# Kernel optimization log

Measured on AMD Instinct MI355X. Metric: run time of the kernel, lower is better.

The kernel has to match this reference:

```python
import jax, jax.numpy as jnp
import numpy as np

N_USERS = 100000
N_ITEMS = 100000
EMB = 64
N_NODES = N_USERS + N_ITEMS + 2  # +1 padding row each for users and items
N_EDGES = 1200000
N_BEHAVIORS = 3
LAYERS = [3, 3, 3]
EPS = 1e-12  # F.normalize eps


def setup_inputs() -> dict:
    key = jax.random.key(0)
    k1, k2, k3, k4, k5 = jax.random.split(key, 5)
    user_emb = jax.random.normal(k1, (N_USERS + 1, EMB), dtype=jnp.float32)
    item_emb = jax.random.normal(k2, (N_ITEMS + 1, EMB), dtype=jnp.float32)
    rows = jax.random.randint(k3, (N_BEHAVIORS, N_EDGES), 0, N_NODES, dtype=jnp.int32)
    cols = jax.random.randint(k4, (N_BEHAVIORS, N_EDGES), 0, N_NODES, dtype=jnp.int32)
    weights = jax.random.uniform(k5, (N_BEHAVIORS, N_EDGES), dtype=jnp.float32)
    return {"user_emb": user_emb, "item_emb": item_emb, "rows": rows,
            "cols": cols, "weights": weights}


def _spmm(rows_b, cols_b, w_b, x):
    # sparse [N,N] @ dense [N,D] via gather + segment-sum (COO SpMM)
    msg = x[cols_b] * w_b[:, None]                      # [E, D]
    return jax.ops.segment_sum(msg, rows_b, num_segments=N_NODES)


def _l2_normalize(x):
    norm = jnp.sqrt(jnp.sum(x * x, axis=-1, keepdims=True))
    return x / jnp.maximum(norm, EPS)


def reference(user_emb, item_emb, rows, cols, weights):
    # NSED.gcn_propagate: sequential LightGCN per behavior with residual chaining
    total = jnp.concatenate([user_emb, item_emb], axis=0)  # [N, D]
    outs = []
    for b in range(N_BEHAVIORS):
        x = total
        acc = x            # running sum of layer embeddings (== mean of stack)
        for _ in range(LAYERS[b]):
            x = _spmm(rows[b], cols[b], weights[b], x)
            acc = acc + x
        lightgcn_emb = acc / jnp.float32(LAYERS[b] + 1)    # stack+mean over layers
        total = _l2_normalize(lightgcn_emb) + total
        outs.append(total)
    return jnp.stack(outs, axis=0)  # [B, N, D]
```

## Files before the change

kernel.cpp:

```cpp
#include <hip/hip_runtime.h>
#include <math.h>

#define N_USERS 100000
#define N_ITEMS 100000
#define EMB 64
#define N_NODES (N_USERS + N_ITEMS + 2)
#define N_EDGES 1200000
#define E3 (3 * N_EDGES)
#define N3 (3 * N_NODES)
#define ND ((long)N_NODES * (long)EMB)

#define KPB 2048
#define NBUCKET ((N3 + KPB - 1) / KPB)
#define CAP 13056
#define EPB 8192
#define SCT 512
#define NB_P1 ((E3 + EPB - 1) / EPB)

typedef float f32x4 __attribute__((ext_vector_type(4)));
typedef float f32x8 __attribute__((ext_vector_type(8)));
typedef unsigned short u16x4 __attribute__((ext_vector_type(4)));
typedef unsigned short u16x8 __attribute__((ext_vector_type(8)));

__device__ inline unsigned short f2bf(float f) {
    unsigned int u = __float_as_uint(f);
    return (unsigned short)((u + 0x7FFFu + ((u >> 16) & 1u)) >> 16);
}
__device__ inline void fma8(f32x8& acc, float w, u16x8 s) {
    #pragma unroll
    for (int j = 0; j < 8; ++j)
        acc[j] = fmaf(w, __uint_as_float((unsigned int)s[j] << 16), acc[j]);
}
__device__ inline f32x8 bf8_to_f8(u16x8 s) {
    f32x8 f;
    #pragma unroll
    for (int j = 0; j < 8; ++j) f[j] = __uint_as_float((unsigned int)s[j] << 16);
    return f;
}
__device__ inline u16x8 f8_to_bf8(f32x8 f) {
    u16x8 s;
    #pragma unroll
    for (int j = 0; j < 8; ++j) s[j] = f2bf(f[j]);
    return s;
}

__global__ void make_tb_kernel(const float4* __restrict__ u,
                               const float4* __restrict__ it,
                               u16x4* __restrict__ tb) {
    long i = (long)blockIdx.x * blockDim.x + threadIdx.x;
    if (i >= ND / 4) return;
    long n = i >> 4;
    float4 v = (n < (long)(N_USERS + 1)) ? u[i] : it[i - (long)(N_USERS + 1) * 16];
    u16x4 b;
    b.x = f2bf(v.x); b.y = f2bf(v.y); b.z = f2bf(v.z); b.w = f2bf(v.w);
    tb[i] = b;
}

__global__ void init_bcur_kernel(int* __restrict__ bcur, unsigned int* __restrict__ sedge) {
    int i = blockIdx.x * blockDim.x + threadIdx.x;
    if (i < NBUCKET) bcur[i] = i * CAP;
    if (i < 16) sedge[E3 + i] = 0u;
}

__global__ void bucket_scatter_kernel(const int* __restrict__ rows,
                                      const int* __restrict__ cols,
                                      const float* __restrict__ w,
                                      int* __restrict__ bcur,
                                      int2* __restrict__ tmpedge) {
    __shared__ int h[NBUCKET];
    __shared__ int lbase[NBUCKET];
    for (int i = threadIdx.x; i < NBUCKET; i += SCT) h[i] = 0;
    __syncthreads();
    long base = (long)blockIdx.x * EPB;
    int keys[EPB / SCT];
    for (int k = 0; k < EPB / SCT; ++k) {
        long e = base + k * SCT + threadIdx.x;
        int key = -1;
        if (e < E3) {
            int b = (e >= 2L * N_EDGES) ? 2 : ((e >= N_EDGES) ? 1 : 0);
            key = b * N_NODES + rows[e];
            atomicAdd(&h[key / KPB], 1);
        }
        keys[k] = key;
    }
    __syncthreads();
    for (int i = threadIdx.x; i < NBUCKET; i += SCT) {
        int c = h[i];
        lbase[i] = c ? atomicAdd(&bcur[i], c) : 0;
        h[i] = 0;
    }
    __syncthreads();
    for (int k = 0; k < EPB / SCT; ++k) {
        long e = base + k * SCT + threadIdx.x;
        int key = keys[k];
        if (key >= 0) {
            int bk = key / KPB;
            int pos = lbase[bk] + atomicAdd(&h[bk], 1);
            int2 pk;
            pk.x = ((key & (KPB - 1)) << 18) | cols[e];
            pk.y = __float_as_int(w[e]);
            tmpedge[pos] = pk;
        }
    }
}

__global__ void bucket_scan_kernel(const int* __restrict__ bcur, int* __restrict__ bbase,
                                   int* __restrict__ rowptr) {
    __shared__ int sm[1024];
    __shared__ int carry;
    int tid = threadIdx.x;
    if (tid == 0) carry = 0;
    __syncthreads();
    for (int base = 0; base < NBUCKET; base += 1024) {
        int i = base + tid;
        int v = (i < NBUCKET) ? (bcur[i] - i * CAP) : 0;
        sm[tid] = v;
        __syncthreads();
        for (int off = 1; off < 1024; off <<= 1) {
            int t = (tid >= off) ? sm[tid - off] : 0;
            __syncthreads();
            sm[tid] += t;
            __syncthreads();
        }
        if (i < NBUCKET) bbase[i] = sm[tid] - v + carry;
        __syncthreads();
        if (tid == 0) carry += sm[1023];
        __syncthreads();
    }
    if (tid == 0) { bbase[NBUCKET] = E3; rowptr[N3] = E3; }
}

__global__ void bucket_sort_kernel(const int* __restrict__ bbase,
                                   const int2* __restrict__ tmpedge,
                                   unsigned int* __restrict__ sedge,
                                   int* __restrict__ rowptr) {
    int g = blockIdx.x;
    int s = bbase[g];
    int cnt = bbase[g + 1] - s;
    long tb = (long)g * CAP;
    __shared__ int h[KPB];
    __shared__ int ex[KPB];
    __shared__ int tmp[512];
    int tid = threadIdx.x;
    #pragma unroll
    for (int j = 0; j < 4; ++j) h[tid * 4 + j] = 0;
    __syncthreads();
    for (int i = tid; i < cnt; i += 512) atomicAdd(&h[tmpedge[tb + i].x >> 18], 1);
    __syncthreads();
    int a0 = h[tid * 4], a1 = h[tid * 4 + 1], a2 = h[tid * 4 + 2], a3 = h[tid * 4 + 3];
    int psum = a0 + a1 + a2 + a3;
    tmp[tid] = psum;
    __syncthreads();
    for (int off = 1; off < 512; off <<= 1) {
        int t = (tid >= off) ? tmp[tid - off] : 0;
        __syncthreads();
        tmp[tid] += t;
        __syncthreads();
    }
    int pex = tmp[tid] - psum;
    ex[tid * 4]     = pex;
    ex[tid * 4 + 1] = pex + a0;
    ex[tid * 4 + 2] = pex + a0 + a1;
    ex[tid * 4 + 3] = pex + a0 + a1 + a2;
    __syncthreads();
    for (int j = tid; j < KPB; j += 512) {
        int key = g * KPB + j;
        if (key < N3) rowptr[key] = s + ex[j];
    }
    #pragma unroll
    for (int j = 0; j < 4; ++j) h[tid * 4 + j] = ex[tid * 4 + j];
    __syncthreads();
    for (int i = tid; i < cnt; i += 512) {
        int2 pk = tmpedge[tb + i];
        int kl = pk.x >> 18;
        int pos = s + atomicAdd(&h[kl], 1);
        float w = __int_as_float(pk.y);
        int wq = (int)fmaf(w, 16384.f, 0.5f);
        wq = wq > 16383 ? 16383 : (wq < 0 ? 0 : wq);
        sedge[pos] = ((unsigned int)(pk.x & 0x3FFFF) << 14) | (unsigned int)wq;
    }
}

__global__ void spmm_bf16_kernel(const int* __restrict__ rowptr,
                                 const unsigned int* __restrict__ sedge,
                                 const u16x8* __restrict__ x,
                                 u16x8* __restrict__ y) {
    int wid  = threadIdx.x >> 6;
    int lane = threadIdx.x & 63;
    int r = lane >> 3;
    int q = lane & 7;
    int n = (blockIdx.x * 4 + wid) * 8 + r;
    if (n >= N_NODES) return;
    int s = rowptr[n], e = rowptr[n + 1];
    f32x8 acc = {0.f, 0.f, 0.f, 0.f, 0.f, 0.f, 0.f, 0.f};
    for (int base = s; ; base += 8) {
        unsigned int ee[8];
        u16x8 bb[8];
        float ww[8];
        #pragma unroll
        for (int j = 0; j < 8; ++j) ee[j] = sedge[base + j];
        #pragma unroll
        for (int j = 0; j < 8; ++j) {
            bool valid = (base + j) < e;
            int c = valid ? (int)(ee[j] >> 14) : 0;
            ww[j] = valid ? (float)(ee[j] & 16383u) * (1.0f / 16384.0f) : 0.f;
            bb[j] = x[(long)c * 8 + q];
        }
        #pragma unroll
        for (int j = 0; j < 8; ++j) fma8(acc, ww[j], bb[j]);
        if (base + 8 >= e) break;
    }
    __builtin_nontemporal_store(f8_to_bf8(acc), &y[(long)n * 8 + q]);
}

__global__ void spmm_final_kernel(const int* __restrict__ rowptr,
                                  const unsigned int* __restrict__ sedge,
                                  const u16x8* __restrict__ Qb,
                                  const float* __restrict__ Tin,
                                  const float* __restrict__ uemb,
                                  const float* __restrict__ iemb,
                                  const u16x8* __restrict__ Pb,
                                  float* __restrict__ outp,
                                  u16x8* __restrict__ TbOut) {
    int wid  = threadIdx.x >> 6;
    int lane = threadIdx.x & 63;
    int r = lane >> 3;
    int q = lane & 7;
    int n = (blockIdx.x * 4 + wid) * 8 + r;
    if (n >= N_NODES) return;
    int s = rowptr[n], e = rowptr[n + 1];
    f32x8 acc = {0.f, 0.f, 0.f, 0.f, 0.f, 0.f, 0.f, 0.f};
    for (int base = s; ; base += 8) {
        unsigned int ee[8];
        u16x8 bb[8];
        float ww[8];
        #pragma unroll
        for (int j = 0; j < 8; ++j) ee[j] = sedge[base + j];
        #pragma unroll
        for (int j = 0; j < 8; ++j) {
            bool valid = (base + j) < e;
            int c = valid ? (int)(ee[j] >> 14) : 0;
            ww[j] = valid ? (float)(ee[j] & 16383u) * (1.0f / 16384.0f) : 0.f;
            bb[j] = Qb[(long)c * 8 + q];
        }
        #pragma unroll
        for (int j = 0; j < 8; ++j) fma8(acc, ww[j], bb[j]);
        if (base + 8 >= e) break;
    }
    const float* tsrc;
    if (Tin) tsrc = Tin + (long)n * EMB;
    else if (n <= N_USERS) tsrc = uemb + (long)n * EMB;
    else tsrc = iemb + (long)(n - N_USERS - 1) * EMB;
    long o = (long)n * 8 + q;
    f32x8 t = *(const f32x8*)(tsrc + q * 8);
    f32x8 p = bf8_to_f8(Pb[o]);
    f32x8 qv = bf8_to_f8(Qb[o]);
    f32x8 v;
    float ss = 0.f;
    #pragma unroll
    for (int j = 0; j < 8; ++j) {
        v[j] = (t[j] + p[j] + qv[j] + acc[j]) * 0.25f;
        ss = fmaf(v[j], v[j], ss);
    }
    ss += __shfl_xor(ss, 1, 64);
    ss += __shfl_xor(ss, 2, 64);
    ss += __shfl_xor(ss, 4, 64);
    float inv = 1.0f / fmaxf(sqrtf(ss), 1e-12f);
    f32x8 ov;
    #pragma unroll
    for (int j = 0; j < 8; ++j) ov[j] = fmaf(v[j], inv, t[j]);
    __builtin_nontemporal_store(ov, (f32x8*)(outp + (long)n * EMB + q * 8));
    if (TbOut) __builtin_nontemporal_store(f8_to_bf8(ov), &TbOut[o]);
}

extern "C" void kernel_launch(void* const* d_in, const int* in_sizes, int n_in,
                              void* d_out, int out_size, void* d_ws, size_t ws_size,
                              hipStream_t stream) {
    const float* user_emb = (const float*)d_in[0];
    const float* item_emb = (const float*)d_in[1];
    const int*   rows     = (const int*)d_in[2];
    const int*   cols     = (const int*)d_in[3];
    const float* weights  = (const float*)d_in[4];
    float* out = (float*)d_out;

    unsigned short* Tb   = (unsigned short*)d_ws;
    unsigned short* Pq   = Tb + ND;
    unsigned short* Qq   = Pq + ND;
    int2* tmpedge = (int2*)(Qq + ND);
    unsigned int* sedge = (unsigned int*)(tmpedge + (long)NBUCKET * CAP);
    int*  rowptr  = (int*)(sedge + E3 + 16);
    int*  bbase   = rowptr + N3 + 2;
    int*  bcur    = bbase + NBUCKET + 2;

    float* o0 = out;
    float* o1 = out + ND;
    float* o2 = out + 2 * ND;

    const long v4_blocks  = (ND / 4 + 255) / 256;
    const long row_blocks = ((long)N_NODES + 31) / 32;

    init_bcur_kernel<<<(NBUCKET + 255) / 256, 256, 0, stream>>>(bcur, sedge);
    bucket_scatter_kernel<<<NB_P1, SCT, 0, stream>>>(rows, cols, weights, bcur, tmpedge);
    bucket_scan_kernel<<<1, 1024, 0, stream>>>(bcur, bbase, rowptr);
    bucket_sort_kernel<<<NBUCKET, 512, 0, stream>>>(bbase, tmpedge, sedge, rowptr);

    make_tb_kernel<<<v4_blocks, 256, 0, stream>>>((const float4*)user_emb,
                                                  (const float4*)item_emb, (u16x4*)Tb);

    const float* Tins[3] = { nullptr, o0, o1 };
    float*       Dsts[3] = { o0, o1, o2 };

    for (int b = 0; b < 3; ++b) {
        const int* rp = rowptr + (long)b * N_NODES;
        u16x8* Pb = (u16x8*)Pq;
        u16x8* Qb = (u16x8*)Qq;

        spmm_bf16_kernel<<<row_blocks, 256, 0, stream>>>(rp, sedge, (const u16x8*)Tb, Pb);
        spmm_bf16_kernel<<<row_blocks, 256, 0, stream>>>(rp, sedge, (const u16x8*)Pb, Qb);
        spmm_final_kernel<<<row_blocks, 256, 0, stream>>>(rp, sedge, (const u16x8*)Qb,
                                                          Tins[b], user_emb, item_emb,
                                                          (const u16x8*)Pb, Dsts[b],
                                                          (b < 2) ? (u16x8*)Tb : nullptr);
    }
}
```

Measured before the change: 417.0 us.

## Replace CSR edge layout with fixed-width ELL plus overflow buffer

Converts the sorted CSR edge list into an ELL layout of 16 slots per row, with edges beyond 16 per row spilled into an atomically allocated overflow buffer. The global bucket-scan kernel goes away because per-row degree and overflow offset are packed into a rowinfo word. SpMM kernels load the 16 ELL records with vector loads and issue all 16 gathers unconditionally, which removes the data-dependent loop for most rows (average degree is about 6). In exchange the kernels always do 16 gathers per row, mostly of zero-weight padding pointing at column 0, and a memset of the ELL array is added. Degree is limited to 1023 by the bit packing and overflow to 1M entries.

```diff
diff --git a/kernel.cpp b/kernel.cpp
--- a/kernel.cpp
+++ b/kernel.cpp
@@ -16,8 +16,9 @@
 #define EPB 8192
 #define SCT 512
 #define NB_P1 ((E3 + EPB - 1) / EPB)
-
-typedef float f32x4 __attribute__((ext_vector_type(4)));
+#define ELLW 16
+#define OVCAP (1 << 20)
+
 typedef float f32x8 __attribute__((ext_vector_type(8)));
 typedef unsigned short u16x4 __attribute__((ext_vector_type(4)));
 typedef unsigned short u16x8 __attribute__((ext_vector_type(8)));
@@ -56,10 +57,10 @@
     tb[i] = b;
 }
 
-__global__ void init_bcur_kernel(int* __restrict__ bcur, unsigned int* __restrict__ sedge) {
-    int i = blockIdx.x * blockDim.x + threadIdx.x;
+__global__ void init_kernel(int* __restrict__ bcur, int* __restrict__ ovcur) {
+    int i = threadIdx.x;
     if (i < NBUCKET) bcur[i] = i * CAP;
-    if (i < 16) sedge[E3 + i] = 0u;
+    if (i == 0) *ovcur = 0;
 }
 
 __global__ void bucket_scatter_kernel(const int* __restrict__ rows,
@@ -104,52 +105,32 @@
     }
 }
 
-__global__ void bucket_scan_kernel(const int* __restrict__ bcur, int* __restrict__ bbase,
-                                   int* __restrict__ rowptr) {
-    __shared__ int sm[1024];
-    __shared__ int carry;
-    int tid = threadIdx.x;
-    if (tid == 0) carry = 0;
-    __syncthreads();
-    for (int base = 0; base < NBUCKET; base += 1024) {
-        int i = base + tid;
-        int v = (i < NBUCKET) ? (bcur[i] - i * CAP) : 0;
-        sm[tid] = v;
-        __syncthreads();
-        for (int off = 1; off < 1024; off <<= 1) {
-            int t = (tid >= off) ? sm[tid - off] : 0;
-            __syncthreads();
-            sm[tid] += t;
-            __syncthreads();
-        }
-        if (i < NBUCKET) bbase[i] = sm[tid] - v + carry;
-        __syncthreads();
-        if (tid == 0) carry += sm[1023];
-        __syncthreads();
-    }
-    if (tid == 0) { bbase[NBUCKET] = E3; rowptr[N3] = E3; }
-}
-
-__global__ void bucket_sort_kernel(const int* __restrict__ bbase,
-                                   const int2* __restrict__ tmpedge,
-                                   unsigned int* __restrict__ sedge,
-                                   int* __restrict__ rowptr) {
+__global__ void bucket_ell_kernel(const int* __restrict__ bcur,
+                                  const int2* __restrict__ tmpedge,
+                                  unsigned int* __restrict__ ell,
+                                  unsigned int* __restrict__ ov,
+                                  unsigned int* __restrict__ rowinfo,
+                                  int* __restrict__ ovcur) {
     int g = blockIdx.x;
-    int s = bbase[g];
-    int cnt = bbase[g + 1] - s;
+    int cnt = bcur[g] - g * CAP;
     long tb = (long)g * CAP;
     __shared__ int h[KPB];
-    __shared__ int ex[KPB];
+    __shared__ int ovs[KPB];
     __shared__ int tmp[512];
+    __shared__ int ovbase_sh;
     int tid = threadIdx.x;
     #pragma unroll
     for (int j = 0; j < 4; ++j) h[tid * 4 + j] = 0;
     __syncthreads();
     for (int i = tid; i < cnt; i += 512) atomicAdd(&h[tmpedge[tb + i].x >> 18], 1);
     __syncthreads();
-    int a0 = h[tid * 4], a1 = h[tid * 4 + 1], a2 = h[tid * 4 + 2], a3 = h[tid * 4 + 3];
-    int psum = a0 + a1 + a2 + a3;
-    tmp[tid] = psum;
+    int c0 = h[tid * 4], c1 = h[tid * 4 + 1], c2 = h[tid * 4 + 2], c3 = h[tid * 4 + 3];
+    int o0 = c0 > ELLW ? c0 - ELLW : 0;
+    int o1 = c1 > ELLW ? c1 - ELLW : 0;
+    int o2 = c2 > ELLW ? c2 - ELLW : 0;
+    int o3 = c3 > ELLW ? c3 - ELLW : 0;
+    int osum = o0 + o1 + o2 + o3;
+    tmp[tid] = osum;
     __syncthreads();
     for (int off = 1; off < 512; off <<= 1) {
         int t = (tid >= off) ? tmp[tid - off] : 0;
@@ -157,32 +138,39 @@
         tmp[tid] += t;
         __syncthreads();
     }
-    int pex = tmp[tid] - psum;
-    ex[tid * 4]     = pex;
-    ex[tid * 4 + 1] = pex + a0;
-    ex[tid * 4 + 2] = pex + a0 + a1;
-    ex[tid * 4 + 3] = pex + a0 + a1 + a2;
-    __syncthreads();
-    for (int j = tid; j < KPB; j += 512) {
-        int key = g * KPB + j;
-        if (key < N3) rowptr[key] = s + ex[j];
-    }
-    #pragma unroll
-    for (int j = 0; j < 4; ++j) h[tid * 4 + j] = ex[tid * 4 + j];
+    if (tid == 511) ovbase_sh = atomicAdd(ovcur, tmp[511]);
+    __syncthreads();
+    int opex = ovbase_sh + tmp[tid] - osum;
+    ovs[tid * 4]     = opex;
+    ovs[tid * 4 + 1] = opex + o0;
+    ovs[tid * 4 + 2] = opex + o0 + o1;
+    ovs[tid * 4 + 3] = opex + o0 + o1 + o2;
+    #pragma unroll
+    for (int j = 0; j < 4; ++j) {
+        int kk = tid * 4 + j;
+        int key = g * KPB + kk;
+        if (key < N3)
+            rowinfo[key] = (unsigned int)h[kk] | ((unsigned int)ovs[kk] << 10);
+        h[kk] = 0;
+    }
     __syncthreads();
     for (int i = tid; i < cnt; i += 512) {
         int2 pk = tmpedge[tb + i];
         int kl = pk.x >> 18;
-        int pos = s + atomicAdd(&h[kl], 1);
+        int slot = atomicAdd(&h[kl], 1);
         float w = __int_as_float(pk.y);
         int wq = (int)fmaf(w, 16384.f, 0.5f);
         wq = wq > 16383 ? 16383 : (wq < 0 ? 0 : wq);
-        sedge[pos] = ((unsigned int)(pk.x & 0x3FFFF) << 14) | (unsigned int)wq;
-    }
-}
-
-__global__ void spmm_bf16_kernel(const int* __restrict__ rowptr,
-                                 const unsigned int* __restrict__ sedge,
+        unsigned int rec = ((unsigned int)(pk.x & 0x3FFFF) << 14) | (unsigned int)wq;
+        long key = (long)g * KPB + kl;
+        if (slot < ELLW) ell[key * ELLW + slot] = rec;
+        else             ov[ovs[kl] + slot - ELLW] = rec;
+    }
+}
+
+__global__ void spmm_bf16_kernel(const unsigned int* __restrict__ ell,
+                                 const unsigned int* __restrict__ rowinfo,
+                                 const unsigned int* __restrict__ ov,
                                  const u16x8* __restrict__ x,
                                  u16x8* __restrict__ y) {
     int wid  = threadIdx.x >> 6;
@@ -191,30 +179,45 @@
     int q = lane & 7;
     int n = (blockIdx.x * 4 + wid) * 8 + r;
     if (n >= N_NODES) return;
-    int s = rowptr[n], e = rowptr[n + 1];
+    const uint4* ep = (const uint4*)(ell + (long)n * ELLW);
+    uint4 v0 = ep[0], v1 = ep[1], v2 = ep[2], v3 = ep[3];
+    unsigned int info = rowinfo[n];
+    unsigned int rec[16] = { v0.x, v0.y, v0.z, v0.w, v1.x, v1.y, v1.z, v1.w,
+                             v2.x, v2.y, v2.z, v2.w, v3.x, v3.y, v3.z, v3.w };
+    u16x8 bb[16];
+    #pragma unroll
+    for (int j = 0; j < 16; ++j) bb[j] = x[(long)(rec[j] >> 14) * 8 + q];
     f32x8 acc = {0.f, 0.f, 0.f, 0.f, 0.f, 0.f, 0.f, 0.f};
-    for (int base = s; ; base += 8) {
-        unsigned int ee[8];
-        u16x8 bb[8];
-        float ww[8];
-        #pragma unroll
-        for (int j = 0; j < 8; ++j) ee[j] = sedge[base + j];
-        #pragma unroll
-        for (int j = 0; j < 8; ++j) {
-            bool valid = (base + j) < e;
-            int c = valid ? (int)(ee[j] >> 14) : 0;
-            ww[j] = valid ? (float)(ee[j] & 16383u) * (1.0f / 16384.0f) : 0.f;
-            bb[j] = x[(long)c * 8 + q];
+    #pragma unroll
+    for (int j = 0; j < 16; ++j)
+        fma8(acc, (float)(rec[j] & 16383u) * (1.0f / 16384.0f), bb[j]);
+    int deg = (int)(info & 1023u);
+    if (deg > ELLW) {
+        int op = (int)(info >> 10);
+        int rem = deg - ELLW;
+        for (int base = 0; base < rem; base += 8) {
+            unsigned int ee[8];
+            u16x8 cb[8];
+            float ww[8];
+            #pragma unroll
+            for (int j = 0; j < 8; ++j) ee[j] = ov[op + base + j];
+            #pragma unroll
+            for (int j = 0; j < 8; ++j) {
+                bool valid = (base + j) < rem;
+                int c = valid ? (int)(ee[j] >> 14) : 0;
+                ww[j] = valid ? (float)(ee[j] & 16383u) * (1.0f / 16384.0f) : 0.f;
+                cb[j] = x[(long)c * 8 + q];
+            }
+            #pragma unroll
+            for (int j = 0; j < 8; ++j) fma8(acc, ww[j], cb[j]);
         }
-        #pragma unroll
-        for (int j = 0; j < 8; ++j) fma8(acc, ww[j], bb[j]);
-        if (base + 8 >= e) break;
     }
     __builtin_nontemporal_store(f8_to_bf8(acc), &y[(long)n * 8 + q]);
 }
 
-__global__ void spmm_final_kernel(const int* __restrict__ rowptr,
-                                  const unsigned int* __restrict__ sedge,
+__global__ void spmm_final_kernel(const unsigned int* __restrict__ ell,
+                                  const unsigned int* __restrict__ rowinfo,
+                                  const unsigned int* __restrict__ ov,
                                   const u16x8* __restrict__ Qb,
                                   const float* __restrict__ Tin,
                                   const float* __restrict__ uemb,
@@ -228,24 +231,38 @@
     int q = lane & 7;
     int n = (blockIdx.x * 4 + wid) * 8 + r;
     if (n >= N_NODES) return;
-    int s = rowptr[n], e = rowptr[n + 1];
+    const uint4* ep = (const uint4*)(ell + (long)n * ELLW);
+    uint4 v0 = ep[0], v1 = ep[1], v2 = ep[2], v3 = ep[3];
+    unsigned int info = rowinfo[n];
+    unsigned int rec[16] = { v0.x, v0.y, v0.z, v0.w, v1.x, v1.y, v1.z, v1.w,
+                             v2.x, v2.y, v2.z, v2.w, v3.x, v3.y, v3.z, v3.w };
+    u16x8 bb[16];
+    #pragma unroll
+    for (int j = 0; j < 16; ++j) bb[j] = Qb[(long)(rec[j] >> 14) * 8 + q];
     f32x8 acc = {0.f, 0.f, 0.f, 0.f, 0.f, 0.f, 0.f, 0.f};
-    for (int base = s; ; base += 8) {
-        unsigned int ee[8];
-        u16x8 bb[8];
-        float ww[8];
-        #pragma unroll
-        for (int j = 0; j < 8; ++j) ee[j] = sedge[base + j];
-        #pragma unroll
-        for (int j = 0; j < 8; ++j) {
-            bool valid = (base + j) < e;
-            int c = valid ? (int)(ee[j] >> 14) : 0;
-            ww[j] = valid ? (float)(ee[j] & 16383u) * (1.0f / 16384.0f) : 0.f;
-            bb[j] = Qb[(long)c * 8 + q];
+    #pragma unroll
+    for (int j = 0; j < 16; ++j)
+        fma8(acc, (float)(rec[j] & 16383u) * (1.0f / 16384.0f), bb[j]);
+    int deg = (int)(info & 1023u);
+    if (deg > ELLW) {
+        int op = (int)(info >> 10);
+        int rem = deg - ELLW;
+        for (int base = 0; base < rem; base += 8) {
+            unsigned int ee[8];
+            u16x8 cb[8];
+            float ww[8];
+            #pragma unroll
+            for (int j = 0; j < 8; ++j) ee[j] = ov[op + base + j];
+            #pragma unroll
+            for (int j = 0; j < 8; ++j) {
+                bool valid = (base + j) < rem;
+                int c = valid ? (int)(ee[j] >> 14) : 0;
+                ww[j] = valid ? (float)(ee[j] & 16383u) * (1.0f / 16384.0f) : 0.f;
+                cb[j] = Qb[(long)c * 8 + q];
+            }
+            #pragma unroll
+            for (int j = 0; j < 8; ++j) fma8(acc, ww[j], cb[j]);
         }
-        #pragma unroll
-        for (int j = 0; j < 8; ++j) fma8(acc, ww[j], bb[j]);
-        if (base + 8 >= e) break;
     }
     const float* tsrc;
     if (Tin) tsrc = Tin + (long)n * EMB;
@@ -266,11 +283,11 @@
     ss += __shfl_xor(ss, 2, 64);
     ss += __shfl_xor(ss, 4, 64);
     float inv = 1.0f / fmaxf(sqrtf(ss), 1e-12f);
-    f32x8 ov;
-    #pragma unroll
-    for (int j = 0; j < 8; ++j) ov[j] = fmaf(v[j], inv, t[j]);
-    __builtin_nontemporal_store(ov, (f32x8*)(outp + (long)n * EMB + q * 8));
-    if (TbOut) __builtin_nontemporal_store(f8_to_bf8(ov), &TbOut[o]);
+    f32x8 ov8;
+    #pragma unroll
+    for (int j = 0; j < 8; ++j) ov8[j] = fmaf(v[j], inv, t[j]);
+    __builtin_nontemporal_store(ov8, (f32x8*)(outp + (long)n * EMB + q * 8));
+    if (TbOut) __builtin_nontemporal_store(f8_to_bf8(ov8), &TbOut[o]);
 }
 
 extern "C" void kernel_launch(void* const* d_in, const int* in_sizes, int n_in,
@@ -287,10 +304,11 @@
     unsigned short* Pq   = Tb + ND;
     unsigned short* Qq   = Pq + ND;
     int2* tmpedge = (int2*)(Qq + ND);
-    unsigned int* sedge = (unsigned int*)(tmpedge + (long)NBUCKET * CAP);
-    int*  rowptr  = (int*)(sedge + E3 + 16);
-    int*  bbase   = rowptr + N3 + 2;
-    int*  bcur    = bbase + NBUCKET + 2;
+    unsigned int* ell     = (unsigned int*)(tmpedge + (long)NBUCKET * CAP);
+    unsigned int* ovbuf   = ell + (long)N3 * ELLW;
+    unsigned int* rowinfo = ovbuf + OVCAP + 16;
+    int* bcur  = (int*)(rowinfo + N3);
+    int* ovcur = bcur + NBUCKET;
 
     float* o0 = out;
     float* o1 = out + ND;
@@ -299,10 +317,11 @@
     const long v4_blocks  = (ND / 4 + 255) / 256;
     const long row_blocks = ((long)N_NODES + 31) / 32;
 
-    init_bcur_kernel<<<(NBUCKET + 255) / 256, 256, 0, stream>>>(bcur, sedge);
+    init_kernel<<<1, 512, 0, stream>>>(bcur, ovcur);
     bucket_scatter_kernel<<<NB_P1, SCT, 0, stream>>>(rows, cols, weights, bcur, tmpedge);
-    bucket_scan_kernel<<<1, 1024, 0, stream>>>(bcur, bbase, rowptr);
-    bucket_sort_kernel<<<NBUCKET, 512, 0, stream>>>(bbase, tmpedge, sedge, rowptr);
+    hipMemsetAsync(ell, 0, (size_t)N3 * ELLW * sizeof(unsigned int), stream);
+    bucket_ell_kernel<<<NBUCKET, 512, 0, stream>>>(bcur, tmpedge, ell, ovbuf,
+                                                   rowinfo, ovcur);
 
     make_tb_kernel<<<v4_blocks, 256, 0, stream>>>((const float4*)user_emb,
                                                   (const float4*)item_emb, (u16x4*)Tb);
@@ -311,13 +330,17 @@
     float*       Dsts[3] = { o0, o1, o2 };
 
     for (int b = 0; b < 3; ++b) {
-        const int* rp = rowptr + (long)b * N_NODES;
+        const unsigned int* el = ell + (long)b * N_NODES * ELLW;
+        const unsigned int* ri = rowinfo + (long)b * N_NODES;
         u16x8* Pb = (u16x8*)Pq;
         u16x8* Qb = (u16x8*)Qq;
 
-        spmm_bf16_kernel<<<row_blocks, 256, 0, stream>>>(rp, sedge, (const u16x8*)Tb, Pb);
-        spmm_bf16_kernel<<<row_blocks, 256, 0, stream>>>(rp, sedge, (const u16x8*)Pb, Qb);
-        spmm_final_kernel<<<row_blocks, 256, 0, stream>>>(rp, sedge, (const u16x8*)Qb,
+        spmm_bf16_kernel<<<row_blocks, 256, 0, stream>>>(el, ri, ovbuf,
+                                                         (const u16x8*)Tb, Pb);
+        spmm_bf16_kernel<<<row_blocks, 256, 0, stream>>>(el, ri, ovbuf,
+                                                         (const u16x8*)Pb, Qb);
+        spmm_final_kernel<<<row_blocks, 256, 0, stream>>>(el, ri, ovbuf,
+                                                          (const u16x8*)Qb,
                                                           Tins[b], user_emb, item_emb,
                                                           (const u16x8*)Pb, Dsts[b],
                                                           (b < 2) ? (u16x8*)Tb : nullptr);
```

Result: slower. 462.4 us (+10.9%).
